# Optimization experiments

Measured on AMD Instinct MI355X. Metric: run time of the kernel, lower is better.

The kernel has to match this reference:

```python
import jax, jax.numpy as jnp
import numpy as np

S = 64.0      # logit scale (self.s)
EMA = 0.99    # margin EMA coefficient; self.m starts at 0 so m_eff = EMA * m_batch


def setup_inputs() -> dict:
    key = jax.random.key(0)
    k1, k2, k3 = jax.random.split(key, 3)
    B, D = 8192, 512
    return {
        "feature1": jax.random.normal(k1, (B, D), dtype=jnp.float32),
        "feature2": jax.random.normal(k2, (B, D), dtype=jnp.float32),
        "label": jax.random.randint(k3, (B,), 0, 4096),
    }


def _l2norm(x):
    return x / jnp.linalg.norm(x, axis=1, keepdims=True)


def reference(feature1, feature2, label):
    B = feature1.shape[0]
    ar = jnp.arange(B)
    f1 = _l2norm(feature1)
    f2 = _l2norm(feature2)
    cos = jnp.clip(f1 @ f2.T, -1.0, 1.0)  # [B, B]
    # The per-label-group loop zeros all same-label off-diagonal entries
    # (the idx_matrix diagonal substitution preserves the true diagonal).
    same_offdiag = (label[:, None] == label[None, :]) & (ar[:, None] != ar[None, :])
    cos = jnp.where(same_offdiag, 0.0, cos)
    # detached margin statistics (clone().detach() / .item())
    clone = jax.lax.stop_gradient(cos)
    pos = clone[ar, ar]                                   # positive cos per row
    neg = jnp.max(clone.at[ar, ar].set(0.0), axis=1)      # hardest negative (sort desc -> max)
    m = EMA * jnp.mean(pos - neg)                         # EMA from self.m = 0
    # m_hot subtracts m at column label (= arange diagonal), then scale
    logits = cos.at[ar, ar].add(-m) * S
    # CrossEntropyLoss with targets arange(B)
    loss = jnp.mean(jax.nn.logsumexp(logits, axis=1) - logits[ar, ar])
    return loss
```

## Files before the change

kernel.cpp:

```cpp
#include <hip/hip_runtime.h>
#include <math.h>

#define BSZ 8192
#define DDIM 512
#define EMA_C 0.99
#define SC 64.0f
#define INV_SC 0.015625f
#define NFINAL 32

typedef _Float16 f16;
typedef _Float16 half8 __attribute__((ext_vector_type(8)));
typedef float f32x4 __attribute__((ext_vector_type(4)));

__device__ __forceinline__ void gload16(const void* g, void* l) {
    __builtin_amdgcn_global_load_lds(
        (const __attribute__((address_space(1))) void*)g,
        (__attribute__((address_space(3))) void*)l, 16, 0, 0);
}

__global__ void prep_kernel(const float* __restrict__ f1,
                            const float* __restrict__ f2,
                            f16* __restrict__ Ah, f16* __restrict__ Al,
                            f16* __restrict__ Bh, f16* __restrict__ Bl,
                            float* __restrict__ stats) {
    if (blockIdx.y == 0 && blockIdx.x < 25) {
        int idx = blockIdx.x * 256 + threadIdx.x;
        if (idx < (3 * BSZ + 4) / 4)
            reinterpret_cast<float4*>(stats)[idx] = make_float4(0.f, 0.f, 0.f, 0.f);
    }
    const int w = threadIdx.x >> 6, l = threadIdx.x & 63;
    const int row = blockIdx.x * 4 + w;
    const float* src = (blockIdx.y == 0) ? f1 : f2;
    f16* dh = (blockIdx.y == 0) ? Ah : Bh;
    f16* dl = (blockIdx.y == 0) ? Al : Bl;
    const float4* p = reinterpret_cast<const float4*>(src + (size_t)row * DDIM);
    float4 v0 = p[l * 2], v1 = p[l * 2 + 1];
    float s = v0.x * v0.x + v0.y * v0.y + v0.z * v0.z + v0.w * v0.w +
              v1.x * v1.x + v1.y * v1.y + v1.z * v1.z + v1.w * v1.w;
#pragma unroll
    for (int off = 32; off; off >>= 1) s += __shfl_xor(s, off);
    const float g = 8.0f / sqrtf(s);
    float x[8] = {v0.x, v0.y, v0.z, v0.w, v1.x, v1.y, v1.z, v1.w};
    half8 h8, l8;
#pragma unroll
    for (int e = 0; e < 8; ++e) {
        float xs = x[e] * g;
        f16 hi = (f16)xs;
        h8[e] = hi;
        l8[e] = (f16)(xs - (float)hi);
    }
    *reinterpret_cast<half8*>(dh + (size_t)row * DDIM + l * 8) = h8;
    *reinterpret_cast<half8*>(dl + (size_t)row * DDIM + l * 8) = l8;
}

__launch_bounds__(256, 2)
__global__ void gemm_pass_kernel(const f16* __restrict__ Ah, const f16* __restrict__ Al,
                                 const f16* __restrict__ Bh, const f16* __restrict__ Bl,
                                 const int* __restrict__ label,
                                 float* __restrict__ pos,
                                 float* __restrict__ negv,
                                 float* __restrict__ Tsum) {
    __shared__ __align__(16) char LDS[49152];
    char* AhL = LDS;
    char* AlL = LDS + 8192;
    char* BhL = LDS + 16384;
    char* BlL = LDS + 32768;

    const int t = threadIdx.x, w = t >> 6, l = t & 63;
    const int rowBase = blockIdx.y * 128;
    const int colBase = blockIdx.x * 256;

    const int kg = (l & 3) ^ ((l >> 3) & 3);
    const int rsub = l >> 2;

    const int qA0 = 2 * w, qA1 = 2 * w + 1;
    const int qB0 = 4 * w, qB1 = 4 * w + 1, qB2 = 4 * w + 2, qB3 = 4 * w + 3;

    const f16* pAh0 = Ah + (size_t)(rowBase + 16 * qA0 + rsub) * DDIM + kg * 8;
    const f16* pAh1 = Ah + (size_t)(rowBase + 16 * qA1 + rsub) * DDIM + kg * 8;
    const f16* pAl0 = Al + (size_t)(rowBase + 16 * qA0 + rsub) * DDIM + kg * 8;
    const f16* pAl1 = Al + (size_t)(rowBase + 16 * qA1 + rsub) * DDIM + kg * 8;
    const f16* pBh0 = Bh + (size_t)(colBase + 16 * qB0 + rsub) * DDIM + kg * 8;
    const f16* pBh1 = Bh + (size_t)(colBase + 16 * qB1 + rsub) * DDIM + kg * 8;
    const f16* pBh2 = Bh + (size_t)(colBase + 16 * qB2 + rsub) * DDIM + kg * 8;
    const f16* pBh3 = Bh + (size_t)(colBase + 16 * qB3 + rsub) * DDIM + kg * 8;
    const f16* pBl0 = Bl + (size_t)(colBase + 16 * qB0 + rsub) * DDIM + kg * 8;
    const f16* pBl1 = Bl + (size_t)(colBase + 16 * qB1 + rsub) * DDIM + kg * 8;
    const f16* pBl2 = Bl + (size_t)(colBase + 16 * qB2 + rsub) * DDIM + kg * 8;
    const f16* pBl3 = Bl + (size_t)(colBase + 16 * qB3 + rsub) * DDIM + kg * 8;

    char* dAh0 = AhL + qA0 * 1024;
    char* dAh1 = AhL + qA1 * 1024;
    char* dAl0 = AlL + qA0 * 1024;
    char* dAl1 = AlL + qA1 * 1024;
    char* dBh0 = BhL + qB0 * 1024;
    char* dBh1 = BhL + qB1 * 1024;
    char* dBh2 = BhL + qB2 * 1024;
    char* dBh3 = BhL + qB3 * 1024;
    char* dBl0 = BlL + qB0 * 1024;
    char* dBl1 = BlL + qB1 * 1024;
    char* dBl2 = BlL + qB2 * 1024;
    char* dBl3 = BlL + qB3 * 1024;

    const int wrow = w >> 1, wcol = w & 1;
    const int ar = l & 15;
    const int ssw = (l >> 4) ^ ((l >> 1) & 3);

    f32x4 acc[4][8];
#pragma unroll
    for (int rt = 0; rt < 4; ++rt)
#pragma unroll
        for (int ct = 0; ct < 8; ++ct) acc[rt][ct] = (f32x4){0.f, 0.f, 0.f, 0.f};

    for (int k0 = 0; k0 < DDIM; k0 += 32) {
        __syncthreads();
        gload16(pAh0 + k0, dAh0);
        gload16(pAh1 + k0, dAh1);
        gload16(pAl0 + k0, dAl0);
        gload16(pAl1 + k0, dAl1);
        gload16(pBh0 + k0, dBh0);
        gload16(pBh1 + k0, dBh1);
        gload16(pBh2 + k0, dBh2);
        gload16(pBh3 + k0, dBh3);
        gload16(pBl0 + k0, dBl0);
        gload16(pBl1 + k0, dBl1);
        gload16(pBl2 + k0, dBl2);
        gload16(pBl3 + k0, dBl3);
        __syncthreads();

        half8 ahf[4], alf[4];
#pragma unroll
        for (int rt = 0; rt < 4; ++rt) {
            const int off = (wrow * 64 + rt * 16 + ar) * 64 + ssw * 16;
            ahf[rt] = *reinterpret_cast<const half8*>(AhL + off);
            alf[rt] = *reinterpret_cast<const half8*>(AlL + off);
        }
#pragma unroll
        for (int ct = 0; ct < 8; ++ct) {
            const int off = (wcol * 128 + ct * 16 + ar) * 64 + ssw * 16;
            half8 bh = *reinterpret_cast<const half8*>(BhL + off);
            half8 bl = *reinterpret_cast<const half8*>(BlL + off);
#pragma unroll
            for (int rt = 0; rt < 4; ++rt) {
                acc[rt][ct] = __builtin_amdgcn_mfma_f32_16x16x32_f16(ahf[rt], bh, acc[rt][ct], 0, 0, 0);
                acc[rt][ct] = __builtin_amdgcn_mfma_f32_16x16x32_f16(ahf[rt], bl, acc[rt][ct], 0, 0, 0);
                acc[rt][ct] = __builtin_amdgcn_mfma_f32_16x16x32_f16(alf[rt], bh, acc[rt][ct], 0, 0, 0);
            }
        }
    }

    const int rowB2 = rowBase + wrow * 64;
    const int colB2 = colBase + wcol * 128;
    const int cl = l & 15, h = l >> 4;

    int lcs[8];
#pragma unroll
    for (int ct = 0; ct < 8; ++ct) lcs[ct] = label[colB2 + ct * 16 + cl];

    float psum[4][4], pmax[4][4];
#pragma unroll
    for (int rt = 0; rt < 4; ++rt)
#pragma unroll
        for (int reg = 0; reg < 4; ++reg) { psum[rt][reg] = 0.f; pmax[rt][reg] = 0.f; }

#pragma unroll
    for (int rt = 0; rt < 4; ++rt) {
        int lr[4];
#pragma unroll
        for (int reg = 0; reg < 4; ++reg) lr[reg] = label[rowB2 + rt * 16 + h * 4 + reg];
#pragma unroll
        for (int ct = 0; ct < 8; ++ct) {
            const int gcol = colB2 + ct * 16 + cl;
#pragma unroll
            for (int reg = 0; reg < 4; ++reg) {
                float v = acc[rt][ct][reg];
                v = fminf(fmaxf(v, -SC), SC);
                const int grow = rowB2 + rt * 16 + h * 4 + reg;
                if (grow == gcol) {
                    pos[grow] = v;
                } else {
                    if (lr[reg] == lcs[ct]) v = 0.0f;
                    psum[rt][reg] += __expf(v);
                    pmax[rt][reg] = fmaxf(pmax[rt][reg], v);
                }
            }
        }
    }

#pragma unroll
    for (int rt = 0; rt < 4; ++rt)
#pragma unroll
        for (int reg = 0; reg < 4; ++reg) {
            float s = psum[rt][reg], mx = pmax[rt][reg];
#pragma unroll
            for (int m = 1; m <= 8; m <<= 1) {
                s += __shfl_xor(s, m);
                mx = fmaxf(mx, __shfl_xor(mx, m));
            }
            if (cl == 0) {
                const int grow = rowB2 + rt * 16 + h * 4 + reg;
                atomicAdd(&Tsum[grow], s);
                atomicMax(reinterpret_cast<int*>(&negv[grow]), __float_as_int(mx));
            }
        }
}

__global__ void final_kernel(const float* __restrict__ pos,
                             const float* __restrict__ negv,
                             const float* __restrict__ Tsum,
                             double* __restrict__ lossAcc,
                             int* __restrict__ ticket,
                             float* __restrict__ out) {
    __shared__ double sd[256];
    const int t = threadIdx.x;

    double s = 0.0;
    for (int i = t; i < BSZ; i += 256) s += (double)pos[i] - (double)negv[i];
    sd[t] = s;
    __syncthreads();
    for (int off = 128; off; off >>= 1) {
        if (t < off) sd[t] += sd[t + off];
        __syncthreads();
    }
    const double mLogit = EMA_C * sd[0] / BSZ;
    __syncthreads();

    const int row = blockIdx.x * 256 + t;
    double d  = (double)pos[row] - mLogit;
    double lt = log((double)Tsum[row]);
    double l;
    if (d >= lt) l = log1p(exp(lt - d));
    else         l = (lt - d) + log1p(exp(d - lt));
    sd[t] = l;
    __syncthreads();
    for (int off = 128; off; off >>= 1) {
        if (t < off) sd[t] += sd[t + off];
        __syncthreads();
    }
    if (t == 0) {
        atomicAdd(lossAcc, sd[0]);
        __threadfence();
        int done = atomicAdd(ticket, 1);
        if (done == NFINAL - 1) {
            double total = atomicAdd(lossAcc, 0.0);
            out[0] = (float)(total / BSZ);
        }
    }
}

extern "C" void kernel_launch(void* const* d_in, const int* in_sizes, int n_in,
                              void* d_out, int out_size, void* d_ws, size_t ws_size,
                              hipStream_t stream) {
    const float* f1    = (const float*)d_in[0];
    const float* f2    = (const float*)d_in[1];
    const int*   label = (const int*)d_in[2];
    float* out = (float*)d_out;

    float* stats = (float*)d_ws;
    float* pos   = stats;
    float* neg   = stats + BSZ;
    float* Tsum  = stats + 2 * BSZ;
    double* lossAcc = (double*)(stats + 3 * BSZ);
    int* ticket  = (int*)(stats + 3 * BSZ + 2);
    f16* Ah = (f16*)((char*)d_ws + 3 * BSZ * sizeof(float) + 16);
    f16* Al = Ah + (size_t)BSZ * DDIM;
    f16* Bh = Al + (size_t)BSZ * DDIM;
    f16* Bl = Bh + (size_t)BSZ * DDIM;

    prep_kernel<<<dim3(BSZ / 4, 2), dim3(256), 0, stream>>>(f1, f2, Ah, Al, Bh, Bl, stats);

    gemm_pass_kernel<<<dim3(BSZ / 256, BSZ / 128), dim3(256), 0, stream>>>(
        Ah, Al, Bh, Bl, label, pos, neg, Tsum);

    final_kernel<<<dim3(NFINAL), dim3(256), 0, stream>>>(pos, neg, Tsum, lossAcc, ticket, out);
}
```

Baseline: 323.6 us.

## Enlarge GEMM tile to 256x256 with double-buffered LDS prefetch

The fused cosine/logsumexp GEMM grows from 128x256 tiles with 256 threads to 256x256 tiles with 512 threads and 8 waves in a 2x4 layout. LDS staging becomes double-buffered: the next k-slice is issued into the alternate buffer while MFMAs consume the current one, which cuts the loop to one barrier per iteration. The aim is to halve redundant global and L2 reads of the A operand and to overlap load latency with compute. The cost is 128 KB of LDS per block, which likely limits residency to one block per CU, and fewer blocks in the grid.

```diff
diff --git a/kernel.cpp b/kernel.cpp
--- a/kernel.cpp
+++ b/kernel.cpp
@@ -5,7 +5,6 @@
 #define DDIM 512
 #define EMA_C 0.99
 #define SC 64.0f
-#define INV_SC 0.015625f
 #define NFINAL 32
 
 typedef _Float16 f16;
@@ -53,123 +52,116 @@
     *reinterpret_cast<half8*>(dl + (size_t)row * DDIM + l * 8) = l8;
 }
 
-__launch_bounds__(256, 2)
+__launch_bounds__(512, 2)
 __global__ void gemm_pass_kernel(const f16* __restrict__ Ah, const f16* __restrict__ Al,
                                  const f16* __restrict__ Bh, const f16* __restrict__ Bl,
                                  const int* __restrict__ label,
                                  float* __restrict__ pos,
                                  float* __restrict__ negv,
                                  float* __restrict__ Tsum) {
-    __shared__ __align__(16) char LDS[49152];
-    char* AhL = LDS;
-    char* AlL = LDS + 8192;
-    char* BhL = LDS + 16384;
-    char* BlL = LDS + 32768;
+    __shared__ __align__(16) char LDS[131072];
 
     const int t = threadIdx.x, w = t >> 6, l = t & 63;
-    const int rowBase = blockIdx.y * 128;
+    const int rowBase = blockIdx.y * 256;
     const int colBase = blockIdx.x * 256;
 
     const int kg = (l & 3) ^ ((l >> 3) & 3);
     const int rsub = l >> 2;
-
-    const int qA0 = 2 * w, qA1 = 2 * w + 1;
-    const int qB0 = 4 * w, qB1 = 4 * w + 1, qB2 = 4 * w + 2, qB3 = 4 * w + 3;
-
-    const f16* pAh0 = Ah + (size_t)(rowBase + 16 * qA0 + rsub) * DDIM + kg * 8;
-    const f16* pAh1 = Ah + (size_t)(rowBase + 16 * qA1 + rsub) * DDIM + kg * 8;
-    const f16* pAl0 = Al + (size_t)(rowBase + 16 * qA0 + rsub) * DDIM + kg * 8;
-    const f16* pAl1 = Al + (size_t)(rowBase + 16 * qA1 + rsub) * DDIM + kg * 8;
-    const f16* pBh0 = Bh + (size_t)(colBase + 16 * qB0 + rsub) * DDIM + kg * 8;
-    const f16* pBh1 = Bh + (size_t)(colBase + 16 * qB1 + rsub) * DDIM + kg * 8;
-    const f16* pBh2 = Bh + (size_t)(colBase + 16 * qB2 + rsub) * DDIM + kg * 8;
-    const f16* pBh3 = Bh + (size_t)(colBase + 16 * qB3 + rsub) * DDIM + kg * 8;
-    const f16* pBl0 = Bl + (size_t)(colBase + 16 * qB0 + rsub) * DDIM + kg * 8;
-    const f16* pBl1 = Bl + (size_t)(colBase + 16 * qB1 + rsub) * DDIM + kg * 8;
-    const f16* pBl2 = Bl + (size_t)(colBase + 16 * qB2 + rsub) * DDIM + kg * 8;
-    const f16* pBl3 = Bl + (size_t)(colBase + 16 * qB3 + rsub) * DDIM + kg * 8;
-
-    char* dAh0 = AhL + qA0 * 1024;
-    char* dAh1 = AhL + qA1 * 1024;
-    char* dAl0 = AlL + qA0 * 1024;
-    char* dAl1 = AlL + qA1 * 1024;
-    char* dBh0 = BhL + qB0 * 1024;
-    char* dBh1 = BhL + qB1 * 1024;
-    char* dBh2 = BhL + qB2 * 1024;
-    char* dBh3 = BhL + qB3 * 1024;
-    char* dBl0 = BlL + qB0 * 1024;
-    char* dBl1 = BlL + qB1 * 1024;
-    char* dBl2 = BlL + qB2 * 1024;
-    char* dBl3 = BlL + qB3 * 1024;
-
-    const int wrow = w >> 1, wcol = w & 1;
+    const int q0 = 2 * w, q1 = 2 * w + 1;
+
+    const f16* gAh0 = Ah + (size_t)(rowBase + 16 * q0 + rsub) * DDIM + kg * 8;
+    const f16* gAh1 = Ah + (size_t)(rowBase + 16 * q1 + rsub) * DDIM + kg * 8;
+    const f16* gAl0 = Al + (size_t)(rowBase + 16 * q0 + rsub) * DDIM + kg * 8;
+    const f16* gAl1 = Al + (size_t)(rowBase + 16 * q1 + rsub) * DDIM + kg * 8;
+    const f16* gBh0 = Bh + (size_t)(colBase + 16 * q0 + rsub) * DDIM + kg * 8;
+    const f16* gBh1 = Bh + (size_t)(colBase + 16 * q1 + rsub) * DDIM + kg * 8;
+    const f16* gBl0 = Bl + (size_t)(colBase + 16 * q0 + rsub) * DDIM + kg * 8;
+    const f16* gBl1 = Bl + (size_t)(colBase + 16 * q1 + rsub) * DDIM + kg * 8;
+
+    const int oAh0 = 0 * 16384 + q0 * 1024, oAh1 = 0 * 16384 + q1 * 1024;
+    const int oAl0 = 1 * 16384 + q0 * 1024, oAl1 = 1 * 16384 + q1 * 1024;
+    const int oBh0 = 2 * 16384 + q0 * 1024, oBh1 = 2 * 16384 + q1 * 1024;
+    const int oBl0 = 3 * 16384 + q0 * 1024, oBl1 = 3 * 16384 + q1 * 1024;
+
+    const int wrow = w >> 2, wcol = w & 3;
     const int ar = l & 15;
     const int ssw = (l >> 4) ^ ((l >> 1) & 3);
 
-    f32x4 acc[4][8];
-#pragma unroll
-    for (int rt = 0; rt < 4; ++rt)
-#pragma unroll
-        for (int ct = 0; ct < 8; ++ct) acc[rt][ct] = (f32x4){0.f, 0.f, 0.f, 0.f};
-
+    f32x4 acc[8][4];
+#pragma unroll
+    for (int rt = 0; rt < 8; ++rt)
+#pragma unroll
+        for (int ct = 0; ct < 4; ++ct) acc[rt][ct] = (f32x4){0.f, 0.f, 0.f, 0.f};
+
+    {
+        char* b = LDS;
+        gload16(gAh0, b + oAh0); gload16(gAh1, b + oAh1);
+        gload16(gAl0, b + oAl0); gload16(gAl1, b + oAl1);
+        gload16(gBh0, b + oBh0); gload16(gBh1, b + oBh1);
+        gload16(gBl0, b + oBl0); gload16(gBl1, b + oBl1);
+    }
+    __syncthreads();
+
+    int cur = 0;
     for (int k0 = 0; k0 < DDIM; k0 += 32) {
+        if (k0 + 32 < DDIM) {
+            char* b = LDS + (cur ^ 1) * 65536;
+            const int ko = k0 + 32;
+            gload16(gAh0 + ko, b + oAh0); gload16(gAh1 + ko, b + oAh1);
+            gload16(gAl0 + ko, b + oAl0); gload16(gAl1 + ko, b + oAl1);
+            gload16(gBh0 + ko, b + oBh0); gload16(gBh1 + ko, b + oBh1);
+            gload16(gBl0 + ko, b + oBl0); gload16(gBl1 + ko, b + oBl1);
+        }
+
+        const char* AhL = LDS + cur * 65536;
+        const char* AlL = AhL + 16384;
+        const char* BhL = AhL + 32768;
+        const char* BlL = AhL + 49152;
+
+        half8 bhf[4], blf[4];
+#pragma unroll
+        for (int ct = 0; ct < 4; ++ct) {
+            const int off = (wcol * 64 + ct * 16 + ar) * 64 + ssw * 16;
+            bhf[ct] = *reinterpret_cast<const half8*>(BhL + off);
+            blf[ct] = *reinterpret_cast<const half8*>(BlL + off);
+        }
+#pragma unroll
+        for (int rt = 0; rt < 8; ++rt) {
+            const int off = (wrow * 128 + rt * 16 + ar) * 64 + ssw * 16;
+            half8 ah = *reinterpret_cast<const half8*>(AhL + off);
+            half8 al = *reinterpret_cast<const half8*>(AlL + off);
+#pragma unroll
+            for (int ct = 0; ct < 4; ++ct) {
+                acc[rt][ct] = __builtin_amdgcn_mfma_f32_16x16x32_f16(ah, bhf[ct], acc[rt][ct], 0, 0, 0);
+                acc[rt][ct] = __builtin_amdgcn_mfma_f32_16x16x32_f16(ah, blf[ct], acc[rt][ct], 0, 0, 0);
+                acc[rt][ct] = __builtin_amdgcn_mfma_f32_16x16x32_f16(al, bhf[ct], acc[rt][ct], 0, 0, 0);
+            }
+        }
         __syncthreads();
-        gload16(pAh0 + k0, dAh0);
-        gload16(pAh1 + k0, dAh1);
-        gload16(pAl0 + k0, dAl0);
-        gload16(pAl1 + k0, dAl1);
-        gload16(pBh0 + k0, dBh0);
-        gload16(pBh1 + k0, dBh1);
-        gload16(pBh2 + k0, dBh2);
-        gload16(pBh3 + k0, dBh3);
-        gload16(pBl0 + k0, dBl0);
-        gload16(pBl1 + k0, dBl1);
-        gload16(pBl2 + k0, dBl2);
-        gload16(pBl3 + k0, dBl3);
-        __syncthreads();
-
-        half8 ahf[4], alf[4];
-#pragma unroll
-        for (int rt = 0; rt < 4; ++rt) {
-            const int off = (wrow * 64 + rt * 16 + ar) * 64 + ssw * 16;
-            ahf[rt] = *reinterpret_cast<const half8*>(AhL + off);
-            alf[rt] = *reinterpret_cast<const half8*>(AlL + off);
-        }
-#pragma unroll
-        for (int ct = 0; ct < 8; ++ct) {
-            const int off = (wcol * 128 + ct * 16 + ar) * 64 + ssw * 16;
-            half8 bh = *reinterpret_cast<const half8*>(BhL + off);
-            half8 bl = *reinterpret_cast<const half8*>(BlL + off);
-#pragma unroll
-            for (int rt = 0; rt < 4; ++rt) {
-                acc[rt][ct] = __builtin_amdgcn_mfma_f32_16x16x32_f16(ahf[rt], bh, acc[rt][ct], 0, 0, 0);
-                acc[rt][ct] = __builtin_amdgcn_mfma_f32_16x16x32_f16(ahf[rt], bl, acc[rt][ct], 0, 0, 0);
-                acc[rt][ct] = __builtin_amdgcn_mfma_f32_16x16x32_f16(alf[rt], bh, acc[rt][ct], 0, 0, 0);
-            }
-        }
-    }
-
-    const int rowB2 = rowBase + wrow * 64;
-    const int colB2 = colBase + wcol * 128;
+        cur ^= 1;
+    }
+
+    const int rowB2 = rowBase + wrow * 128;
+    const int colB2 = colBase + wcol * 64;
     const int cl = l & 15, h = l >> 4;
 
-    int lcs[8];
-#pragma unroll
-    for (int ct = 0; ct < 8; ++ct) lcs[ct] = label[colB2 + ct * 16 + cl];
-
-    float psum[4][4], pmax[4][4];
-#pragma unroll
-    for (int rt = 0; rt < 4; ++rt)
+    int lcs[4];
+#pragma unroll
+    for (int ct = 0; ct < 4; ++ct) lcs[ct] = label[colB2 + ct * 16 + cl];
+
+    float psum[8][4], pmax[8][4];
+#pragma unroll
+    for (int rt = 0; rt < 8; ++rt)
 #pragma unroll
         for (int reg = 0; reg < 4; ++reg) { psum[rt][reg] = 0.f; pmax[rt][reg] = 0.f; }
 
 #pragma unroll
-    for (int rt = 0; rt < 4; ++rt) {
+    for (int rt = 0; rt < 8; ++rt) {
         int lr[4];
 #pragma unroll
         for (int reg = 0; reg < 4; ++reg) lr[reg] = label[rowB2 + rt * 16 + h * 4 + reg];
 #pragma unroll
-        for (int ct = 0; ct < 8; ++ct) {
+        for (int ct = 0; ct < 4; ++ct) {
             const int gcol = colB2 + ct * 16 + cl;
 #pragma unroll
             for (int reg = 0; reg < 4; ++reg) {
@@ -188,7 +180,7 @@
     }
 
 #pragma unroll
-    for (int rt = 0; rt < 4; ++rt)
+    for (int rt = 0; rt < 8; ++rt)
 #pragma unroll
         for (int reg = 0; reg < 4; ++reg) {
             float s = psum[rt][reg], mx = pmax[rt][reg];
@@ -269,7 +261,7 @@
 
     prep_kernel<<<dim3(BSZ / 4, 2), dim3(256), 0, stream>>>(f1, f2, Ah, Al, Bh, Bl, stats);
 
-    gemm_pass_kernel<<<dim3(BSZ / 256, BSZ / 128), dim3(256), 0, stream>>>(
+    gemm_pass_kernel<<<dim3(BSZ / 256, BSZ / 256), dim3(512), 0, stream>>>(
         Ah, Al, Bh, Bl, label, pos, neg, Tsum);
 
     final_kernel<<<dim3(NFINAL), dim3(256), 0, stream>>>(pos, neg, Tsum, lossAcc, ticket, out);
```

Measured after the change: 371.0 us. 1.15x slower.
